# Kernel tuning notes

Hardware: AMD Instinct MI355X
Metric: run time of the kernel (lower is better)

Reference implementation:

```python
import jax, jax.numpy as jnp
import numpy as np

N_HEAD = 16

def setup_inputs() -> dict:
    key = jax.random.key(0)
    ks = jax.random.split(key, 7)
    B, T, C = 2, 2048, 1024
    return {
        "query": jax.random.normal(ks[0], (B, T, C), jnp.float32),
        "key": jax.random.normal(ks[1], (B, T, C), jnp.float32),
        "value": jax.random.normal(ks[2], (B, T, C), jnp.float32),
        "Wq": jax.random.normal(ks[3], (C, C), jnp.float32) * (1.0 / np.sqrt(C)),
        "Wk": jax.random.normal(ks[4], (C, C), jnp.float32) * (1.0 / np.sqrt(C)),
        "Wv": jax.random.normal(ks[5], (C, C), jnp.float32) * (1.0 / np.sqrt(C)),
        "Wo": jax.random.normal(ks[6], (C, C), jnp.float32) * (1.0 / np.sqrt(C)),
    }

def reference(query, key, value, Wq, Wk, Wv, Wo):
    B, T, C = query.shape
    H = N_HEAD
    D = C // H
    # QKV projections (torch Linear: x @ W.T, no bias)
    q = (query @ Wq.T).reshape(B, T, H, D).transpose(0, 2, 1, 3)  # [B,H,T,D]
    k = (key   @ Wk.T).reshape(B, T, H, D).transpose(0, 2, 1, 3)
    v = (value @ Wv.T).reshape(B, T, H, D).transpose(0, 2, 1, 3)
    scale = 1.0 / np.sqrt(D).astype(np.float32)
    att = jnp.einsum("bhqd,bhkd->bhqk", q, k) * scale  # [B,H,T,T]
    att = jax.nn.softmax(att, axis=-1)
    y = jnp.einsum("bhqk,bhkd->bhqd", att, v)  # [B,H,T,D]
    y = y.transpose(0, 2, 1, 3).reshape(B, T, C)
    return y @ Wo.T
```

## Files before the change

### kernel.cpp

```cpp
#include <hip/hip_runtime.h>
#include <hip/hip_bf16.h>
#include <cstdint>

typedef __attribute__((ext_vector_type(8))) short bf16x8;
typedef __attribute__((ext_vector_type(4))) float f32x4;
typedef __attribute__((ext_vector_type(16))) float f32x16;
typedef __attribute__((ext_vector_type(4))) unsigned short us4;

#define MFMA16(a, b, c) __builtin_amdgcn_mfma_f32_16x16x32_bf16((a), (b), (c), 0, 0, 0)
#define MFMA32(a, b, c) __builtin_amdgcn_mfma_f32_32x32x16_bf16((a), (b), (c), 0, 0, 0)
#define GLB_PTR(p) ((const __attribute__((address_space(1))) void*)(p))
#define LDS_PTR(p) ((__attribute__((address_space(3))) void*)(p))
#define WAITV(n) asm volatile("s_waitcnt vmcnt(" #n ")" ::: "memory")

__device__ __forceinline__ unsigned short f2bf(float f) {
    union { float f; unsigned u; } v; v.f = f;
    unsigned r = v.u + 0x7fffu + ((v.u >> 16) & 1u);
    return (unsigned short)(r >> 16);
}

__device__ __forceinline__ unsigned cvtpk(float lo, float hi) {
    unsigned r;
    asm("v_cvt_pk_bf16_f32 %0, %1, %2" : "=v"(r) : "v"(lo), "v"(hi));
    return r;
}

struct CastArgs {
    const float* src[7];
    unsigned short* dst[7];
    int n4[7];
};

__global__ __launch_bounds__(256) void cast_f32_bf16(CastArgs a) {
    const int id = blockIdx.y;
    const float4* s = (const float4*)a.src[id];
    us4* d = (us4*)a.dst[id];
    const int n4 = a.n4[id];
    for (int i = blockIdx.x * blockDim.x + threadIdx.x; i < n4;
         i += gridDim.x * blockDim.x) {
        float4 v = s[i];
        us4 o;
        o.x = f2bf(v.x); o.y = f2bf(v.y); o.z = f2bf(v.z); o.w = f2bf(v.w);
        d[i] = o;
    }
}

struct GemmGroup {
    const unsigned short* A[3];
    const unsigned short* B[3];
    unsigned short* C[3];
};

__global__ __launch_bounds__(256, 2)
void gemm_qkv(GemmGroup gg, int M, int N, int K) {
    __shared__ __align__(16) unsigned short As[3][128 * 32];
    __shared__ __align__(16) unsigned short Bs[3][128 * 32];
    const int z = blockIdx.z;
    const unsigned short* __restrict__ A = gg.A[z];
    const unsigned short* __restrict__ B = gg.B[z];
    unsigned short* __restrict__ C = gg.C[z];
    const int t = threadIdx.x;
    const int lane = t & 63, wave = t >> 6;
    const int row0 = blockIdx.x * 128, col0 = blockIdx.y * 128;
    const int wr = (wave >> 1) * 64, wc = (wave & 1) * 64;
    const int r = lane & 15, g = lane >> 4;
    const int srow = t >> 2;
    const int scol = (t & 3) * 8;

#define GSTAGE(sl, k0)                                                         \
    {                                                                          \
        _Pragma("unroll")                                                      \
        for (int i = 0; i < 2; ++i) {                                          \
            const int rr = i * 64 + srow;                                      \
            __builtin_amdgcn_global_load_lds(                                  \
                GLB_PTR(A + (size_t)(row0 + rr) * K + (k0) + scol),            \
                LDS_PTR(&As[sl][rr * 32 + scol]), 16, 0, 0);                   \
            __builtin_amdgcn_global_load_lds(                                  \
                GLB_PTR(B + (size_t)(col0 + rr) * K + (k0) + scol),            \
                LDS_PTR(&Bs[sl][rr * 32 + scol]), 16, 0, 0);                   \
        }                                                                      \
    }

    f32x4 acc[4][4] = {};
    GSTAGE(0, 0);
    GSTAGE(1, 32);

    for (int it = 0; it < 32; ++it) {
        if (it < 31) WAITV(4); else WAITV(0);
        __builtin_amdgcn_s_barrier();
        __builtin_amdgcn_sched_barrier(0);
        if (it + 2 < 32) GSTAGE((it + 2) % 3, (it + 2) * 32);
        const int sl = it % 3;
        bf16x8 a[4], b[4];
#pragma unroll
        for (int m = 0; m < 4; ++m)
            a[m] = *(const bf16x8*)(&As[sl][(wr + m * 16 + r) * 32 + g * 8]);
#pragma unroll
        for (int n = 0; n < 4; ++n)
            b[n] = *(const bf16x8*)(&Bs[sl][(wc + n * 16 + r) * 32 + g * 8]);
        __builtin_amdgcn_s_setprio(1);
#pragma unroll
        for (int m = 0; m < 4; ++m)
#pragma unroll
            for (int n = 0; n < 4; ++n)
                acc[m][n] = MFMA16(a[m], b[n], acc[m][n]);
        __builtin_amdgcn_s_setprio(0);
    }
#undef GSTAGE

    const float sc = (z == 0) ? 0.18033688011112042f : 1.0f;
#pragma unroll
    for (int m = 0; m < 4; ++m) {
#pragma unroll
        for (int n = 0; n < 4; ++n) {
#pragma unroll
            for (int i = 0; i < 4; ++i) {
                const int row = row0 + wr + m * 16 + g * 4 + i;
                const int col = col0 + wc + n * 16 + r;
                const int b_ = row >> 11, tt = row & 2047;
                const int h = col >> 6, d = col & 63;
                const int bh = b_ * 16 + h;
                size_t idx;
                if (z == 2) {
                    const int l = (d & 31) + 32 * ((tt >> 3) & 1);
                    idx = ((((size_t)(bh * 32 + (tt >> 6))) * 2 + (d >> 5)) * 4 +
                           ((tt >> 4) & 3)) * 512 + l * 8 + (tt & 7);
                } else {
                    const int l = (tt & 31) + 32 * ((d >> 3) & 1);
                    idx = (((size_t)(bh * 64 + (tt >> 5))) * 4 + (d >> 4)) * 512 +
                          l * 8 + (d & 7);
                }
                C[idx] = f2bf(acc[m][n][i] * sc);
            }
        }
    }
}

__global__ __launch_bounds__(256, 2)
void gemm_wo(const unsigned short* __restrict__ A,
             const unsigned short* __restrict__ B,
             float* __restrict__ C, int M, int N, int K) {
    __shared__ __align__(16) unsigned short As[3][64 * 32];
    __shared__ __align__(16) unsigned short Bs[3][128 * 32];
    const int t = threadIdx.x;
    const int lane = t & 63, wave = t >> 6;
    const int row0 = blockIdx.x * 64, col0 = blockIdx.y * 128;
    const int wc = wave * 32;
    const int r = lane & 15, g = lane >> 4;
    const int srow = t >> 2;
    const int scol = (t & 3) * 8;

#define WSTAGE(sl, k0)                                                         \
    {                                                                          \
        __builtin_amdgcn_global_load_lds(                                      \
            GLB_PTR(A + (size_t)(row0 + srow) * K + (k0) + scol),              \
            LDS_PTR(&As[sl][srow * 32 + scol]), 16, 0, 0);                     \
        _Pragma("unroll")                                                      \
        for (int i = 0; i < 2; ++i) {                                          \
            const int rr = i * 64 + srow;                                      \
            __builtin_amdgcn_global_load_lds(                                  \
                GLB_PTR(B + (size_t)(col0 + rr) * K + (k0) + scol),            \
                LDS_PTR(&Bs[sl][rr * 32 + scol]), 16, 0, 0);                   \
        }                                                                      \
    }

    f32x4 acc[4][2] = {};
    WSTAGE(0, 0);
    WSTAGE(1, 32);

    for (int it = 0; it < 32; ++it) {
        if (it < 31) WAITV(3); else WAITV(0);
        __builtin_amdgcn_s_barrier();
        __builtin_amdgcn_sched_barrier(0);
        if (it + 2 < 32) WSTAGE((it + 2) % 3, (it + 2) * 32);
        const int sl = it % 3;
        bf16x8 a[4], b[2];
#pragma unroll
        for (int m = 0; m < 4; ++m)
            a[m] = *(const bf16x8*)(&As[sl][(m * 16 + r) * 32 + g * 8]);
#pragma unroll
        for (int n = 0; n < 2; ++n)
            b[n] = *(const bf16x8*)(&Bs[sl][(wc + n * 16 + r) * 32 + g * 8]);
        __builtin_amdgcn_s_setprio(1);
#pragma unroll
        for (int m = 0; m < 4; ++m)
#pragma unroll
            for (int n = 0; n < 2; ++n)
                acc[m][n] = MFMA16(a[m], b[n], acc[m][n]);
        __builtin_amdgcn_s_setprio(0);
    }
#undef WSTAGE

#pragma unroll
    for (int m = 0; m < 4; ++m)
#pragma unroll
        for (int n = 0; n < 2; ++n)
#pragma unroll
            for (int i = 0; i < 4; ++i) {
                const int row = row0 + m * 16 + g * 4 + i;
                const int col = col0 + wc + n * 16 + r;
                C[(size_t)row * N + col] = acc[m][n][i];
            }
}

__global__ __launch_bounds__(256, 2)
void attn_fwd(const unsigned short* __restrict__ Qpk,
              const unsigned short* __restrict__ Kpk,
              const unsigned short* __restrict__ Vpk,
              unsigned short* __restrict__ Y) {
    __shared__ __align__(16) unsigned short kv_lds[4][16][512];
    const int t = threadIdx.x, lane = t & 63, w = t >> 6;
    const int q31 = lane & 31, hi = lane >> 5;

    const int flat = blockIdx.x;
    const int swz = (flat & 7) * 64 + (flat >> 3);
    const int qt = swz & 15, bh = swz >> 4;
    const int qb0 = qt * 128;

    const unsigned short* Qb = Qpk + ((size_t)(bh * 64 + qt * 4 + w)) * 2048;
    const unsigned short* Kb = Kpk + (size_t)bh * 131072;
    const unsigned short* Vb = Vpk + (size_t)bh * 131072;

    bf16x8 qf[4];
#pragma unroll
    for (int s = 0; s < 4; ++s)
        qf[s] = *(const bf16x8*)(Qb + s * 512 + lane * 8);
    WAITV(0);

    f32x16 o0 = {}, o1 = {};
    float l_ = 0.f;

#define STAGE(sl, kv0)                                                         \
    {                                                                          \
        _Pragma("unroll")                                                      \
        for (int i = 0; i < 4; ++i) {                                          \
            const int f = w * 4 + i;                                           \
            const unsigned short* src =                                        \
                (f < 8 ? Kb : Vb) + (kv0) * 64 + (f & 7) * 512 + lane * 8;     \
            __builtin_amdgcn_global_load_lds(                                  \
                GLB_PTR(src), LDS_PTR(&kv_lds[sl][f][lane * 8]), 16, 0, 0);    \
        }                                                                      \
    }

    STAGE(0, 0);
    STAGE(1, 64);
    STAGE(2, 128);

    for (int it = 0; it < 32; ++it) {
        if (it < 30) WAITV(8);
        else if (it == 30) WAITV(4);
        else WAITV(0);
        __builtin_amdgcn_s_barrier();
        __builtin_amdgcn_sched_barrier(0);
        if (it + 3 < 32) STAGE((it + 3) & 3, (it + 3) * 64);
        const int sl = it & 3;

        bf16x8 kf[8];
#pragma unroll
        for (int i = 0; i < 8; ++i)
            kf[i] = *(const bf16x8*)(&kv_lds[sl][i][lane * 8]);
        f32x16 s0, s1;
#pragma unroll
        for (int r = 0; r < 16; ++r) { s0[r] = -12.f; s1[r] = -12.f; }
        __builtin_amdgcn_s_setprio(1);
#pragma unroll
        for (int s = 0; s < 4; ++s) s0 = MFMA32(kf[s], qf[s], s0);
#pragma unroll
        for (int s = 0; s < 4; ++s) s1 = MFMA32(kf[4 + s], qf[s], s1);
        __builtin_amdgcn_s_setprio(0);

        float p[32];
#pragma unroll
        for (int r = 0; r < 16; ++r) p[r] = __builtin_amdgcn_exp2f(s0[r]);
#pragma unroll
        for (int r = 0; r < 16; ++r) p[16 + r] = __builtin_amdgcn_exp2f(s1[r]);

        float sm[16];
#pragma unroll
        for (int r = 0; r < 16; ++r) sm[r] = p[r] + p[16 + r];
#pragma unroll
        for (int d = 8; d > 0; d >>= 1)
#pragma unroll
            for (int r = 0; r < d; ++r) sm[r] += sm[r + d];
        l_ += sm[0] + __shfl_xor(sm[0], 32);

        unsigned c[16];
#pragma unroll
        for (int i = 0; i < 16; ++i) c[i] = cvtpk(p[2 * i], p[2 * i + 1]);

        bf16x8 vf[8];
#pragma unroll
        for (int i = 0; i < 8; ++i)
            vf[i] = *(const bf16x8*)(&kv_lds[sl][8 + i][lane * 8]);

        __builtin_amdgcn_s_setprio(1);
#pragma unroll
        for (int s = 0; s < 4; ++s) {
            const int base = (s >> 1) * 8 + (s & 1) * 4;
            unsigned a0 = c[base + 0], b0 = c[base + 2];
            unsigned a1 = c[base + 1], b1 = c[base + 3];
            asm volatile("v_permlane32_swap_b32 %0, %1" : "+v"(a0), "+v"(b0));
            asm volatile("v_permlane32_swap_b32 %0, %1" : "+v"(a1), "+v"(b1));
            union { unsigned u[4]; bf16x8 v; } pb;
            pb.u[0] = a0; pb.u[1] = a1; pb.u[2] = b0; pb.u[3] = b1;
            o0 = MFMA32(vf[s], pb.v, o0);
            o1 = MFMA32(vf[4 + s], pb.v, o1);
        }
        __builtin_amdgcn_s_setprio(0);
    }
#undef STAGE

    __syncthreads();

    unsigned short (*yb)[68] = (unsigned short (*)[68])kv_lds;
    const float rinv = 1.0f / l_;
#pragma unroll
    for (int r = 0; r < 16; ++r) {
        const int dd = (r & 3) + 8 * (r >> 2) + 4 * hi;
        yb[w * 32 + q31][dd] = f2bf(o0[r] * rinv);
        yb[w * 32 + q31][32 + dd] = f2bf(o1[r] * rinv);
    }
    __syncthreads();
    const int b_ = bh >> 4, h = bh & 15;
#pragma unroll
    for (int i = 0; i < 8; ++i) {
        const int row = i * 16 + (t >> 4);
        const int col = (t & 15) * 4;
        *(us4*)(Y + ((size_t)(b_ * 2048 + qb0 + row)) * 1024 + h * 64 + col) =
            *(const us4*)(&yb[row][col]);
    }
}

extern "C" void kernel_launch(void* const* d_in, const int* in_sizes, int n_in,
                              void* d_out, int out_size, void* d_ws, size_t ws_size,
                              hipStream_t stream) {
    uint8_t* ws = (uint8_t*)d_ws;
    unsigned short* xq = (unsigned short*)(ws + 0);
    unsigned short* xk = (unsigned short*)(ws + 8388608);
    unsigned short* xv = (unsigned short*)(ws + 16777216);
    unsigned short* wq = (unsigned short*)(ws + 25165824);
    unsigned short* wk = (unsigned short*)(ws + 27262976);
    unsigned short* wv = (unsigned short*)(ws + 29360128);
    unsigned short* wo = (unsigned short*)(ws + 31457280);
    unsigned short* Qp = (unsigned short*)(ws + 33554432);
    unsigned short* Kp = (unsigned short*)(ws + 41943040);
    unsigned short* Vp = (unsigned short*)(ws + 50331648);
    unsigned short* y  = xq;

    CastArgs ca;
    ca.src[0] = (const float*)d_in[0]; ca.dst[0] = xq; ca.n4[0] = 4194304 / 4;
    ca.src[1] = (const float*)d_in[1]; ca.dst[1] = xk; ca.n4[1] = 4194304 / 4;
    ca.src[2] = (const float*)d_in[2]; ca.dst[2] = xv; ca.n4[2] = 4194304 / 4;
    ca.src[3] = (const float*)d_in[3]; ca.dst[3] = wq; ca.n4[3] = 1048576 / 4;
    ca.src[4] = (const float*)d_in[4]; ca.dst[4] = wk; ca.n4[4] = 1048576 / 4;
    ca.src[5] = (const float*)d_in[5]; ca.dst[5] = wv; ca.n4[5] = 1048576 / 4;
    ca.src[6] = (const float*)d_in[6]; ca.dst[6] = wo; ca.n4[6] = 1048576 / 4;
    cast_f32_bf16<<<dim3(512, 7), 256, 0, stream>>>(ca);

    GemmGroup gg;
    gg.A[0] = xq; gg.B[0] = wq; gg.C[0] = Qp;
    gg.A[1] = xk; gg.B[1] = wk; gg.C[1] = Kp;
    gg.A[2] = xv; gg.B[2] = wv; gg.C[2] = Vp;
    gemm_qkv<<<dim3(32, 8, 3), 256, 0, stream>>>(gg, 4096, 1024, 1024);

    attn_fwd<<<dim3(512), 256, 0, stream>>>(Qp, Kp, Vp, y);

    gemm_wo<<<dim3(64, 8), 256, 0, stream>>>(y, wo, (float*)d_out, 4096, 1024, 1024);
}
```

Before: 123.8 us.

## Process two query tiles per wave in attention to reuse K/V fragments

```diff
diff --git a/kernel.cpp b/kernel.cpp
--- a/kernel.cpp
+++ b/kernel.cpp
@@ -203,7 +203,7 @@
             }
 }
 
-__global__ __launch_bounds__(256, 2)
+__global__ __launch_bounds__(256, 1)
 void attn_fwd(const unsigned short* __restrict__ Qpk,
               const unsigned short* __restrict__ Kpk,
               const unsigned short* __restrict__ Vpk,
@@ -213,22 +213,24 @@
     const int q31 = lane & 31, hi = lane >> 5;
 
     const int flat = blockIdx.x;
-    const int swz = (flat & 7) * 64 + (flat >> 3);
-    const int qt = swz & 15, bh = swz >> 4;
-    const int qb0 = qt * 128;
-
-    const unsigned short* Qb = Qpk + ((size_t)(bh * 64 + qt * 4 + w)) * 2048;
+    const int swz = (flat & 7) * 32 + (flat >> 3);
+    const int qt = swz & 7, bh = swz >> 3;
+    const int qb0 = qt * 256;
+
+    const unsigned short* Qb = Qpk + ((size_t)(bh * 64 + qt * 8 + w * 2)) * 2048;
     const unsigned short* Kb = Kpk + (size_t)bh * 131072;
     const unsigned short* Vb = Vpk + (size_t)bh * 131072;
 
-    bf16x8 qf[4];
-#pragma unroll
-    for (int s = 0; s < 4; ++s)
-        qf[s] = *(const bf16x8*)(Qb + s * 512 + lane * 8);
+    bf16x8 qfA[4], qfB[4];
+#pragma unroll
+    for (int s = 0; s < 4; ++s) {
+        qfA[s] = *(const bf16x8*)(Qb + s * 512 + lane * 8);
+        qfB[s] = *(const bf16x8*)(Qb + 2048 + s * 512 + lane * 8);
+    }
     WAITV(0);
 
-    f32x16 o0 = {}, o1 = {};
-    float l_ = 0.f;
+    f32x16 oA0 = {}, oA1 = {}, oB0 = {}, oB1 = {};
+    float lA = 0.f, lB = 0.f;
 
 #define STAGE(sl, kv0)                                                         \
     {                                                                          \
@@ -259,22 +261,26 @@
 #pragma unroll
         for (int i = 0; i < 8; ++i)
             kf[i] = *(const bf16x8*)(&kv_lds[sl][i][lane * 8]);
-        f32x16 s0, s1;
-#pragma unroll
-        for (int r = 0; r < 16; ++r) { s0[r] = -12.f; s1[r] = -12.f; }
-        __builtin_amdgcn_s_setprio(1);
-#pragma unroll
-        for (int s = 0; s < 4; ++s) s0 = MFMA32(kf[s], qf[s], s0);
-#pragma unroll
-        for (int s = 0; s < 4; ++s) s1 = MFMA32(kf[4 + s], qf[s], s1);
-        __builtin_amdgcn_s_setprio(0);
+
+        f32x16 sA0, sA1, sB0, sB1;
+#pragma unroll
+        for (int r = 0; r < 16; ++r) {
+            sA0[r] = -12.f; sA1[r] = -12.f; sB0[r] = -12.f; sB1[r] = -12.f;
+        }
+#pragma unroll
+        for (int s = 0; s < 4; ++s) sA0 = MFMA32(kf[s], qfA[s], sA0);
+#pragma unroll
+        for (int s = 0; s < 4; ++s) sA1 = MFMA32(kf[4 + s], qfA[s], sA1);
+#pragma unroll
+        for (int s = 0; s < 4; ++s) sB0 = MFMA32(kf[s], qfB[s], sB0);
+#pragma unroll
+        for (int s = 0; s < 4; ++s) sB1 = MFMA32(kf[4 + s], qfB[s], sB1);
 
         float p[32];
 #pragma unroll
-        for (int r = 0; r < 16; ++r) p[r] = __builtin_amdgcn_exp2f(s0[r]);
-#pragma unroll
-        for (int r = 0; r < 16; ++r) p[16 + r] = __builtin_amdgcn_exp2f(s1[r]);
-
+        for (int r = 0; r < 16; ++r) p[r] = __builtin_amdgcn_exp2f(sA0[r]);
+#pragma unroll
+        for (int r = 0; r < 16; ++r) p[16 + r] = __builtin_amdgcn_exp2f(sA1[r]);
         float sm[16];
 #pragma unroll
         for (int r = 0; r < 16; ++r) sm[r] = p[r] + p[16 + r];
@@ -282,48 +288,77 @@
         for (int d = 8; d > 0; d >>= 1)
 #pragma unroll
             for (int r = 0; r < d; ++r) sm[r] += sm[r + d];
-        l_ += sm[0] + __shfl_xor(sm[0], 32);
-
-        unsigned c[16];
-#pragma unroll
-        for (int i = 0; i < 16; ++i) c[i] = cvtpk(p[2 * i], p[2 * i + 1]);
+        lA += sm[0] + __shfl_xor(sm[0], 32);
+
+        unsigned cA[16];
+#pragma unroll
+        for (int i = 0; i < 16; ++i) cA[i] = cvtpk(p[2 * i], p[2 * i + 1]);
 
         bf16x8 vf[8];
 #pragma unroll
         for (int i = 0; i < 8; ++i)
             vf[i] = *(const bf16x8*)(&kv_lds[sl][8 + i][lane * 8]);
 
-        __builtin_amdgcn_s_setprio(1);
 #pragma unroll
         for (int s = 0; s < 4; ++s) {
             const int base = (s >> 1) * 8 + (s & 1) * 4;
-            unsigned a0 = c[base + 0], b0 = c[base + 2];
-            unsigned a1 = c[base + 1], b1 = c[base + 3];
+            unsigned a0 = cA[base + 0], b0 = cA[base + 2];
+            unsigned a1 = cA[base + 1], b1 = cA[base + 3];
             asm volatile("v_permlane32_swap_b32 %0, %1" : "+v"(a0), "+v"(b0));
             asm volatile("v_permlane32_swap_b32 %0, %1" : "+v"(a1), "+v"(b1));
             union { unsigned u[4]; bf16x8 v; } pb;
             pb.u[0] = a0; pb.u[1] = a1; pb.u[2] = b0; pb.u[3] = b1;
-            o0 = MFMA32(vf[s], pb.v, o0);
-            o1 = MFMA32(vf[4 + s], pb.v, o1);
+            oA0 = MFMA32(vf[s], pb.v, oA0);
+            oA1 = MFMA32(vf[4 + s], pb.v, oA1);
         }
-        __builtin_amdgcn_s_setprio(0);
+
+#pragma unroll
+        for (int r = 0; r < 16; ++r) p[r] = __builtin_amdgcn_exp2f(sB0[r]);
+#pragma unroll
+        for (int r = 0; r < 16; ++r) p[16 + r] = __builtin_amdgcn_exp2f(sB1[r]);
+#pragma unroll
+        for (int r = 0; r < 16; ++r) sm[r] = p[r] + p[16 + r];
+#pragma unroll
+        for (int d = 8; d > 0; d >>= 1)
+#pragma unroll
+            for (int r = 0; r < d; ++r) sm[r] += sm[r + d];
+        lB += sm[0] + __shfl_xor(sm[0], 32);
+
+        unsigned cB[16];
+#pragma unroll
+        for (int i = 0; i < 16; ++i) cB[i] = cvtpk(p[2 * i], p[2 * i + 1]);
+
+#pragma unroll
+        for (int s = 0; s < 4; ++s) {
+            const int base = (s >> 1) * 8 + (s & 1) * 4;
+            unsigned a0 = cB[base + 0], b0 = cB[base + 2];
+            unsigned a1 = cB[base + 1], b1 = cB[base + 3];
+            asm volatile("v_permlane32_swap_b32 %0, %1" : "+v"(a0), "+v"(b0));
+            asm volatile("v_permlane32_swap_b32 %0, %1" : "+v"(a1), "+v"(b1));
+            union { unsigned u[4]; bf16x8 v; } pb;
+            pb.u[0] = a0; pb.u[1] = a1; pb.u[2] = b0; pb.u[3] = b1;
+            oB0 = MFMA32(vf[s], pb.v, oB0);
+            oB1 = MFMA32(vf[4 + s], pb.v, oB1);
+        }
     }
 #undef STAGE
 
     __syncthreads();
 
     unsigned short (*yb)[68] = (unsigned short (*)[68])kv_lds;
-    const float rinv = 1.0f / l_;
+    const float riA = 1.0f / lA, riB = 1.0f / lB;
 #pragma unroll
     for (int r = 0; r < 16; ++r) {
         const int dd = (r & 3) + 8 * (r >> 2) + 4 * hi;
-        yb[w * 32 + q31][dd] = f2bf(o0[r] * rinv);
-        yb[w * 32 + q31][32 + dd] = f2bf(o1[r] * rinv);
+        yb[w * 64 + q31][dd] = f2bf(oA0[r] * riA);
+        yb[w * 64 + q31][32 + dd] = f2bf(oA1[r] * riA);
+        yb[w * 64 + 32 + q31][dd] = f2bf(oB0[r] * riB);
+        yb[w * 64 + 32 + q31][32 + dd] = f2bf(oB1[r] * riB);
     }
     __syncthreads();
     const int b_ = bh >> 4, h = bh & 15;
 #pragma unroll
-    for (int i = 0; i < 8; ++i) {
+    for (int i = 0; i < 16; ++i) {
         const int row = i * 16 + (t >> 4);
         const int col = (t & 15) * 4;
         *(us4*)(Y + ((size_t)(b_ * 2048 + qb0 + row)) * 1024 + h * 64 + col) =
@@ -363,7 +398,7 @@
     gg.A[2] = xv; gg.B[2] = wv; gg.C[2] = Vp;
     gemm_qkv<<<dim3(32, 8, 3), 256, 0, stream>>>(gg, 4096, 1024, 1024);
 
-    attn_fwd<<<dim3(512), 256, 0, stream>>>(Qp, Kp, Vp, y);
+    attn_fwd<<<dim3(256), 256, 0, stream>>>(Qp, Kp, Vp, y);
 
     gemm_wo<<<dim3(64, 8), 256, 0, stream>>>(y, wo, (float*)d_out, 4096, 1024, 1024);
 }
```

After: 127.3 us. 2.8% more time.

## Fuse activation fp32-to-bf16 cast into QKV GEMM and stage outputs via LDS

Applied to the files above, without the earlier changes.

```diff
diff --git a/kernel.cpp b/kernel.cpp
--- a/kernel.cpp
+++ b/kernel.cpp
@@ -12,6 +12,7 @@
 #define GLB_PTR(p) ((const __attribute__((address_space(1))) void*)(p))
 #define LDS_PTR(p) ((__attribute__((address_space(3))) void*)(p))
 #define WAITV(n) asm volatile("s_waitcnt vmcnt(" #n ")" ::: "memory")
+#define WAITLGKM asm volatile("s_waitcnt lgkmcnt(0)" ::: "memory")
 
 __device__ __forceinline__ unsigned short f2bf(float f) {
     union { float f; unsigned u; } v; v.f = f;
@@ -26,17 +27,15 @@
 }
 
 struct CastArgs {
-    const float* src[7];
-    unsigned short* dst[7];
-    int n4[7];
+    const float* src[4];
+    unsigned short* dst[4];
 };
 
-__global__ __launch_bounds__(256) void cast_f32_bf16(CastArgs a) {
+__global__ __launch_bounds__(256) void cast_w(CastArgs a) {
     const int id = blockIdx.y;
     const float4* s = (const float4*)a.src[id];
     us4* d = (us4*)a.dst[id];
-    const int n4 = a.n4[id];
-    for (int i = blockIdx.x * blockDim.x + threadIdx.x; i < n4;
+    for (int i = blockIdx.x * blockDim.x + threadIdx.x; i < 262144;
          i += gridDim.x * blockDim.x) {
         float4 v = s[i];
         us4 o;
@@ -46,67 +45,112 @@
 }
 
 struct GemmGroup {
-    const unsigned short* A[3];
+    const float* A[3];
     const unsigned short* B[3];
     unsigned short* C[3];
 };
 
 __global__ __launch_bounds__(256, 2)
-void gemm_qkv(GemmGroup gg, int M, int N, int K) {
-    __shared__ __align__(16) unsigned short As[3][128 * 32];
-    __shared__ __align__(16) unsigned short Bs[3][128 * 32];
-    const int z = blockIdx.z;
-    const unsigned short* __restrict__ A = gg.A[z];
+void gemm_qkv(GemmGroup gg) {
+    __shared__ __align__(16) unsigned short lds[24576];
+    const int t = threadIdx.x;
+    const int lane = t & 63, wave = t >> 6;
+
+    const int flat = blockIdx.x;
+    const int work = (flat & 7) * 96 + (flat >> 3);
+    const int x = work / 96, j = work % 96;
+    const int bx = x * 4 + (j & 3), by = (j >> 2) & 7, z = j >> 5;
+
+    const float* __restrict__ A = gg.A[z];
     const unsigned short* __restrict__ B = gg.B[z];
     unsigned short* __restrict__ C = gg.C[z];
-    const int t = threadIdx.x;
-    const int lane = t & 63, wave = t >> 6;
-    const int row0 = blockIdx.x * 128, col0 = blockIdx.y * 128;
+    const int row0 = bx * 128, col0 = by * 128;
     const int wr = (wave >> 1) * 64, wc = (wave & 1) * 64;
     const int r = lane & 15, g = lane >> 4;
-    const int srow = t >> 2;
-    const int scol = (t & 3) * 8;
-
-#define GSTAGE(sl, k0)                                                         \
-    {                                                                          \
-        _Pragma("unroll")                                                      \
-        for (int i = 0; i < 2; ++i) {                                          \
-            const int rr = i * 64 + srow;                                      \
+    const int arow = t >> 1, acol = (t & 1) * 16;
+    const int srow = t >> 2, scol = (t & 3) * 8;
+
+#define AS(sl) (&lds[(sl) * 4096])
+#define BS(sl) (&lds[12288 + (sl) * 4096])
+
+#define ALOAD(fa, k0)                                                          \
+    {                                                                          \
+        _Pragma("unroll")                                                      \
+        for (int jj = 0; jj < 4; ++jj)                                         \
+            fa[jj] = *(const float4*)(A + (size_t)(row0 + arow) * 1024 +       \
+                                      (k0) + acol + jj * 4);                   \
+    }
+#define BGLD(sl, k0)                                                           \
+    {                                                                          \
+        _Pragma("unroll")                                                      \
+        for (int jj = 0; jj < 2; ++jj) {                                       \
+            const int rr = jj * 64 + srow;                                     \
             __builtin_amdgcn_global_load_lds(                                  \
-                GLB_PTR(A + (size_t)(row0 + rr) * K + (k0) + scol),            \
-                LDS_PTR(&As[sl][rr * 32 + scol]), 16, 0, 0);                   \
-            __builtin_amdgcn_global_load_lds(                                  \
-                GLB_PTR(B + (size_t)(col0 + rr) * K + (k0) + scol),            \
-                LDS_PTR(&Bs[sl][rr * 32 + scol]), 16, 0, 0);                   \
+                GLB_PTR(B + (size_t)(col0 + rr) * 1024 + (k0) + scol),         \
+                LDS_PTR(BS(sl) + rr * 32 + scol), 16, 0, 0);                   \
         }                                                                      \
     }
+#define AWRITE(fa, sl)                                                         \
+    {                                                                          \
+        _Pragma("unroll")                                                      \
+        for (int jj = 0; jj < 2; ++jj) {                                       \
+            uint4 wv;                                                          \
+            wv.x = cvtpk(fa[2 * jj].x, fa[2 * jj].y);                          \
+            wv.y = cvtpk(fa[2 * jj].z, fa[2 * jj].w);                          \
+            wv.z = cvtpk(fa[2 * jj + 1].x, fa[2 * jj + 1].y);                  \
+            wv.w = cvtpk(fa[2 * jj + 1].z, fa[2 * jj + 1].w);                  \
+            *(uint4*)(AS(sl) + arow * 32 + acol + jj * 8) = wv;                \
+        }                                                                      \
+    }
+#define COMPUTE(sl)                                                            \
+    {                                                                          \
+        bf16x8 af[4], bf[4];                                                   \
+        _Pragma("unroll")                                                      \
+        for (int m = 0; m < 4; ++m)                                            \
+            af[m] = *(const bf16x8*)(AS(sl) + (wr + m * 16 + r) * 32 + g * 8); \
+        _Pragma("unroll")                                                      \
+        for (int n = 0; n < 4; ++n)                                            \
+            bf[n] = *(const bf16x8*)(BS(sl) + (wc + n * 16 + r) * 32 + g * 8); \
+        __builtin_amdgcn_s_setprio(1);                                         \
+        _Pragma("unroll")                                                      \
+        for (int m = 0; m < 4; ++m)                                            \
+            _Pragma("unroll")                                                  \
+            for (int n = 0; n < 4; ++n)                                        \
+                acc[m][n] = MFMA16(af[m], bf[n], acc[m][n]);                   \
+        __builtin_amdgcn_s_setprio(0);                                         \
+    }
+#define BODY(it, FA_L, FA_W)                                                   \
+    {                                                                          \
+        if ((it) + 2 < 32) {                                                   \
+            ALOAD(FA_L, ((it) + 2) * 32);                                      \
+            BGLD(((it) + 2) % 3, ((it) + 2) * 32);                             \
+        }                                                                      \
+        COMPUTE((it) % 3);                                                     \
+        if ((it) < 30) WAITV(6); else WAITV(0);                                \
+        if ((it) < 31) AWRITE(FA_W, ((it) + 1) % 3);                           \
+        WAITLGKM;                                                              \
+        __builtin_amdgcn_s_barrier();                                          \
+    }
 
     f32x4 acc[4][4] = {};
-    GSTAGE(0, 0);
-    GSTAGE(1, 32);
-
-    for (int it = 0; it < 32; ++it) {
-        if (it < 31) WAITV(4); else WAITV(0);
-        __builtin_amdgcn_s_barrier();
-        __builtin_amdgcn_sched_barrier(0);
-        if (it + 2 < 32) GSTAGE((it + 2) % 3, (it + 2) * 32);
-        const int sl = it % 3;
-        bf16x8 a[4], b[4];
-#pragma unroll
-        for (int m = 0; m < 4; ++m)
-            a[m] = *(const bf16x8*)(&As[sl][(wr + m * 16 + r) * 32 + g * 8]);
-#pragma unroll
-        for (int n = 0; n < 4; ++n)
-            b[n] = *(const bf16x8*)(&Bs[sl][(wc + n * 16 + r) * 32 + g * 8]);
-        __builtin_amdgcn_s_setprio(1);
-#pragma unroll
-        for (int m = 0; m < 4; ++m)
-#pragma unroll
-            for (int n = 0; n < 4; ++n)
-                acc[m][n] = MFMA16(a[m], b[n], acc[m][n]);
-        __builtin_amdgcn_s_setprio(0);
-    }
-#undef GSTAGE
+    float4 fa0[4], fa1[4];
+
+    ALOAD(fa0, 0); BGLD(0, 0);
+    ALOAD(fa1, 32); BGLD(1, 32);
+    WAITV(6);
+    AWRITE(fa0, 0);
+    WAITLGKM;
+    __builtin_amdgcn_s_barrier();
+
+    for (int t2 = 0; t2 < 32; t2 += 2) {
+        BODY(t2, fa0, fa1);
+        BODY(t2 + 1, fa1, fa0);
+    }
+#undef BODY
+#undef COMPUTE
+#undef AWRITE
+#undef BGLD
+#undef ALOAD
 
     const float sc = (z == 0) ? 0.18033688011112042f : 1.0f;
 #pragma unroll
@@ -115,24 +159,35 @@
         for (int n = 0; n < 4; ++n) {
 #pragma unroll
             for (int i = 0; i < 4; ++i) {
-                const int row = row0 + wr + m * 16 + g * 4 + i;
-                const int col = col0 + wc + n * 16 + r;
-                const int b_ = row >> 11, tt = row & 2047;
-                const int h = col >> 6, d = col & 63;
-                const int bh = b_ * 16 + h;
-                size_t idx;
+                const int lr = wr + m * 16 + g * 4 + i;
+                const int cl = wc + n * 16 + r;
+                const int hl = cl >> 6, d = cl & 63;
+                int off;
                 if (z == 2) {
-                    const int l = (d & 31) + 32 * ((tt >> 3) & 1);
-                    idx = ((((size_t)(bh * 32 + (tt >> 6))) * 2 + (d >> 5)) * 4 +
-                           ((tt >> 4) & 3)) * 512 + l * 8 + (tt & 7);
+                    const int l = (d & 31) + 32 * ((lr >> 3) & 1);
+                    off = hl * 8192 + (lr >> 6) * 4096 + (d >> 5) * 2048 +
+                          ((lr >> 4) & 3) * 512 + l * 8 + (lr & 7);
                 } else {
-                    const int l = (tt & 31) + 32 * ((d >> 3) & 1);
-                    idx = (((size_t)(bh * 64 + (tt >> 5))) * 4 + (d >> 4)) * 512 +
+                    const int l = (lr & 31) + 32 * ((d >> 3) & 1);
+                    off = hl * 8192 + (lr >> 5) * 2048 + ((d >> 4) & 3) * 512 +
                           l * 8 + (d & 7);
                 }
-                C[idx] = f2bf(acc[m][n][i] * sc);
+                lds[off] = f2bf(acc[m][n][i] * sc);
             }
         }
+    }
+    __syncthreads();
+    const int b_ = row0 >> 11, h0 = by * 2;
+    const int tg0 = (row0 & 2047) >> 5, v0 = (row0 & 2047) >> 6;
+#pragma unroll
+    for (int hl = 0; hl < 2; ++hl) {
+        const size_t gb = (z == 2)
+            ? ((size_t)(((b_ * 16 + h0 + hl) * 32 + v0) * 2)) * 2048
+            : ((size_t)((b_ * 16 + h0 + hl) * 64 + tg0)) * 2048;
+        const uint4* src = (const uint4*)&lds[hl * 8192];
+        uint4* dst = (uint4*)&C[gb];
+#pragma unroll
+        for (int k = 0; k < 4; ++k) dst[t + k * 256] = src[t + k * 256];
     }
 }
 
@@ -335,33 +390,27 @@
                               void* d_out, int out_size, void* d_ws, size_t ws_size,
                               hipStream_t stream) {
     uint8_t* ws = (uint8_t*)d_ws;
-    unsigned short* xq = (unsigned short*)(ws + 0);
-    unsigned short* xk = (unsigned short*)(ws + 8388608);
-    unsigned short* xv = (unsigned short*)(ws + 16777216);
-    unsigned short* wq = (unsigned short*)(ws + 25165824);
-    unsigned short* wk = (unsigned short*)(ws + 27262976);
-    unsigned short* wv = (unsigned short*)(ws + 29360128);
-    unsigned short* wo = (unsigned short*)(ws + 31457280);
-    unsigned short* Qp = (unsigned short*)(ws + 33554432);
-    unsigned short* Kp = (unsigned short*)(ws + 41943040);
-    unsigned short* Vp = (unsigned short*)(ws + 50331648);
-    unsigned short* y  = xq;
+    unsigned short* y  = (unsigned short*)(ws + 0);
+    unsigned short* wq = (unsigned short*)(ws + 8388608);
+    unsigned short* wk = (unsigned short*)(ws + 10485760);
+    unsigned short* wv = (unsigned short*)(ws + 12582912);
+    unsigned short* wo = (unsigned short*)(ws + 14680064);
+    unsigned short* Qp = (unsigned short*)(ws + 16777216);
+    unsigned short* Kp = (unsigned short*)(ws + 25165824);
+    unsigned short* Vp = (unsigned short*)(ws + 33554432);
 
     CastArgs ca;
-    ca.src[0] = (const float*)d_in[0]; ca.dst[0] = xq; ca.n4[0] = 4194304 / 4;
-    ca.src[1] = (const float*)d_in[1]; ca.dst[1] = xk; ca.n4[1] = 4194304 / 4;
-    ca.src[2] = (const float*)d_in[2]; ca.dst[2] = xv; ca.n4[2] = 4194304 / 4;
-    ca.src[3] = (const float*)d_in[3]; ca.dst[3] = wq; ca.n4[3] = 1048576 / 4;
-    ca.src[4] = (const float*)d_in[4]; ca.dst[4] = wk; ca.n4[4] = 1048576 / 4;
-    ca.src[5] = (const float*)d_in[5]; ca.dst[5] = wv; ca.n4[5] = 1048576 / 4;
-    ca.src[6] = (const float*)d_in[6]; ca.dst[6] = wo; ca.n4[6] = 1048576 / 4;
-    cast_f32_bf16<<<dim3(512, 7), 256, 0, stream>>>(ca);
+    ca.src[0] = (const float*)d_in[3]; ca.dst[0] = wq;
+    ca.src[1] = (const float*)d_in[4]; ca.dst[1] = wk;
+    ca.src[2] = (const float*)d_in[5]; ca.dst[2] = wv;
+    ca.src[3] = (const float*)d_in[6]; ca.dst[3] = wo;
+    cast_w<<<dim3(64, 4), 256, 0, stream>>>(ca);
 
     GemmGroup gg;
-    gg.A[0] = xq; gg.B[0] = wq; gg.C[0] = Qp;
-    gg.A[1] = xk; gg.B[1] = wk; gg.C[1] = Kp;
-    gg.A[2] = xv; gg.B[2] = wv; gg.C[2] = Vp;
-    gemm_qkv<<<dim3(32, 8, 3), 256, 0, stream>>>(gg, 4096, 1024, 1024);
+    gg.A[0] = (const float*)d_in[0]; gg.B[0] = wq; gg.C[0] = Qp;
+    gg.A[1] = (const float*)d_in[1]; gg.B[1] = wk; gg.C[1] = Kp;
+    gg.A[2] = (const float*)d_in[2]; gg.B[2] = wv; gg.C[2] = Vp;
+    gemm_qkv<<<dim3(768), 256, 0, stream>>>(gg);
 
     attn_fwd<<<dim3(512), 256, 0, stream>>>(Qp, Kp, Vp, y);
 
```

Result: faster. 119.5 us (-3.5%).

## Software-pipeline QK^T of next KV tile with softmax of current tile

Applied to the files above, without the earlier changes.

```diff
diff --git a/kernel.cpp b/kernel.cpp
--- a/kernel.cpp
+++ b/kernel.cpp
@@ -246,34 +246,51 @@
     STAGE(1, 64);
     STAGE(2, 128);
 
+    WAITV(8);
+    __builtin_amdgcn_s_barrier();
+    __builtin_amdgcn_sched_barrier(0);
+    f32x16 sA0, sA1;
+    {
+        bf16x8 kf[8];
+#pragma unroll
+        for (int i = 0; i < 8; ++i)
+            kf[i] = *(const bf16x8*)(&kv_lds[0][i][lane * 8]);
+#pragma unroll
+        for (int r = 0; r < 16; ++r) { sA0[r] = -12.f; sA1[r] = -12.f; }
+        __builtin_amdgcn_s_setprio(1);
+#pragma unroll
+        for (int s = 0; s < 4; ++s) sA0 = MFMA32(kf[s], qf[s], sA0);
+#pragma unroll
+        for (int s = 0; s < 4; ++s) sA1 = MFMA32(kf[4 + s], qf[s], sA1);
+        __builtin_amdgcn_s_setprio(0);
+    }
+
     for (int it = 0; it < 32; ++it) {
-        if (it < 30) WAITV(8);
-        else if (it == 30) WAITV(4);
-        else WAITV(0);
+        if (it < 30) WAITV(4); else WAITV(0);
         __builtin_amdgcn_s_barrier();
         __builtin_amdgcn_sched_barrier(0);
         if (it + 3 < 32) STAGE((it + 3) & 3, (it + 3) * 64);
-        const int sl = it & 3;
-
-        bf16x8 kf[8];
-#pragma unroll
-        for (int i = 0; i < 8; ++i)
-            kf[i] = *(const bf16x8*)(&kv_lds[sl][i][lane * 8]);
-        f32x16 s0, s1;
-#pragma unroll
-        for (int r = 0; r < 16; ++r) { s0[r] = -12.f; s1[r] = -12.f; }
-        __builtin_amdgcn_s_setprio(1);
-#pragma unroll
-        for (int s = 0; s < 4; ++s) s0 = MFMA32(kf[s], qf[s], s0);
-#pragma unroll
-        for (int s = 0; s < 4; ++s) s1 = MFMA32(kf[4 + s], qf[s], s1);
-        __builtin_amdgcn_s_setprio(0);
+
+        f32x16 sN0, sN1;
+        if (it + 1 < 32) {
+            const int sln = (it + 1) & 3;
+            bf16x8 kf[8];
+#pragma unroll
+            for (int i = 0; i < 8; ++i)
+                kf[i] = *(const bf16x8*)(&kv_lds[sln][i][lane * 8]);
+#pragma unroll
+            for (int r = 0; r < 16; ++r) { sN0[r] = -12.f; sN1[r] = -12.f; }
+#pragma unroll
+            for (int s = 0; s < 4; ++s) sN0 = MFMA32(kf[s], qf[s], sN0);
+#pragma unroll
+            for (int s = 0; s < 4; ++s) sN1 = MFMA32(kf[4 + s], qf[s], sN1);
+        }
 
         float p[32];
 #pragma unroll
-        for (int r = 0; r < 16; ++r) p[r] = __builtin_amdgcn_exp2f(s0[r]);
-#pragma unroll
-        for (int r = 0; r < 16; ++r) p[16 + r] = __builtin_amdgcn_exp2f(s1[r]);
+        for (int r = 0; r < 16; ++r) p[r] = __builtin_amdgcn_exp2f(sA0[r]);
+#pragma unroll
+        for (int r = 0; r < 16; ++r) p[16 + r] = __builtin_amdgcn_exp2f(sA1[r]);
 
         float sm[16];
 #pragma unroll
@@ -288,6 +305,7 @@
 #pragma unroll
         for (int i = 0; i < 16; ++i) c[i] = cvtpk(p[2 * i], p[2 * i + 1]);
 
+        const int sl = it & 3;
         bf16x8 vf[8];
 #pragma unroll
         for (int i = 0; i < 8; ++i)
@@ -307,6 +325,9 @@
             o1 = MFMA32(vf[4 + s], pb.v, o1);
         }
         __builtin_amdgcn_s_setprio(0);
+
+        sA0 = sN0;
+        sA1 = sN1;
     }
 #undef STAGE
 
```

New measurement: 123.1 us, median of 2. No clear change (-0.6%).
